# Performance work log

Measured on AMD Instinct MI355X. Metric: run time of the kernel, lower is better.

Reference implementation:

```python
import jax, jax.numpy as jnp
import numpy as np

HID = 64

def _rnn_layer(x, W_ih, W_hh, b_ih, b_hh):
    # x: [B, T, F]; PyTorch RNN step: h_t = tanh(x_t @ W_ih.T + b_ih + h_{t-1} @ W_hh.T + b_hh)
    # Precompute the input projection for all timesteps as one big GEMM.
    x_proj = jnp.einsum('btf,hf->bth', x, W_ih) + b_ih  # [B, T, H]
    B = x.shape[0]
    h0 = jnp.zeros((B, HID), x.dtype)

    def step(h, xt):
        h = jnp.tanh(xt + h @ W_hh.T + b_hh)
        return h, h

    _, hs = jax.lax.scan(step, h0, jnp.swapaxes(x_proj, 0, 1))  # hs: [T, B, H]
    return jnp.swapaxes(hs, 0, 1)  # [B, T, H]


def setup_inputs() -> dict:
    key = jax.random.key(0)
    ks = jax.random.split(key, 20)
    B, T, F = 4096, 128, 14
    s_in = 1.0 / np.sqrt(HID)  # PyTorch RNN init scale
    d = {
        'x': jax.random.normal(ks[0], (B, T, F), jnp.float32),
        'W_ih0': jax.random.normal(ks[1], (HID, F), jnp.float32) * s_in,
        'W_hh0': jax.random.normal(ks[2], (HID, HID), jnp.float32) * s_in,
        'b_ih0': jax.random.normal(ks[3], (HID,), jnp.float32) * s_in,
        'b_hh0': jax.random.normal(ks[4], (HID,), jnp.float32) * s_in,
        'W_ih1': jax.random.normal(ks[5], (HID, HID), jnp.float32) * s_in,
        'W_hh1': jax.random.normal(ks[6], (HID, HID), jnp.float32) * s_in,
        'b_ih1': jax.random.normal(ks[7], (HID,), jnp.float32) * s_in,
        'b_hh1': jax.random.normal(ks[8], (HID,), jnp.float32) * s_in,
        'W_ih2': jax.random.normal(ks[9], (HID, HID), jnp.float32) * s_in,
        'W_hh2': jax.random.normal(ks[10], (HID, HID), jnp.float32) * s_in,
        'b_ih2': jax.random.normal(ks[11], (HID,), jnp.float32) * s_in,
        'b_hh2': jax.random.normal(ks[12], (HID,), jnp.float32) * s_in,
        'fc1_w': jax.random.normal(ks[13], (32, HID), jnp.float32) * s_in,
        'fc1_b': jax.random.normal(ks[14], (32,), jnp.float32) * s_in,
        'fc2_w': jax.random.normal(ks[15], (1, 32), jnp.float32) * (1.0 / np.sqrt(32)),
        'fc2_b': jax.random.normal(ks[16], (1,), jnp.float32) * (1.0 / np.sqrt(32)),
    }
    return d


def reference(x, W_ih0, W_hh0, b_ih0, b_hh0, W_ih1, W_hh1, b_ih1, b_hh1,
              W_ih2, W_hh2, b_ih2, b_hh2, fc1_w, fc1_b, fc2_w, fc2_b):
    h = _rnn_layer(x, W_ih0, W_hh0, b_ih0, b_hh0)
    h = _rnn_layer(h, W_ih1, W_hh1, b_ih1, b_hh1)
    h = _rnn_layer(h, W_ih2, W_hh2, b_ih2, b_hh2)
    last = h[:, -1, :]                       # [B, H]
    y = jax.nn.relu(last @ fc1_w.T + fc1_b)  # [B, 32]
    return y @ fc2_w.T + fc2_b               # [B, 1]
```

## Files before the change

kernel.cpp:

```cpp
#include <hip/hip_runtime.h>

typedef short  s16x8 __attribute__((ext_vector_type(8)));
typedef float  f32x4 __attribute__((ext_vector_type(4)));
typedef float  f32x2 __attribute__((ext_vector_type(2)));
typedef unsigned int u32;
typedef unsigned int u32x4 __attribute__((ext_vector_type(4)));
typedef unsigned short u16;

#define DEVI static __device__ __forceinline__

#if __has_builtin(__builtin_amdgcn_exp2f)
#define EXP2(v) __builtin_amdgcn_exp2f(v)
#else
#define EXP2(v) exp2f(v)
#endif

constexpr int T_  = 128;
constexpr int F_  = 14;
constexpr int H_  = 64;
constexpr int BPB = 16;
constexpr int K_  = 4;
constexpr int NCH = T_ / K_;

constexpr int HF_BYTES   = 2 * 2 * K_ * 2 * 64 * 16;
constexpr int XBUF_BYTES = 2 * K_ * 64 * 16;
constexpr int QBUF_BYTES = 2 * 3 * K_ * 4 * 64 * 16;
constexpr int SMEM_BYTES = HF_BYTES + XBUF_BYTES + QBUF_BYTES;

DEVI u16 f2bf(float f) {
  u32 u = __builtin_bit_cast(u32, f);
  u += 0x7fffu + ((u >> 16) & 1u);
  return (u16)(u >> 16);
}
DEVI u32 cvtpk(float a, float b) {
  u32 r;
  asm("v_cvt_pk_bf16_f32 %0, %1, %2" : "=v"(r) : "v"(a), "v"(b));
  return r;
}
DEVI s16x8 packfrag(const f32x4& a, const f32x4& b) {
  u32x4 p;
  p[0] = cvtpk(a[0], a[1]); p[1] = cvtpk(a[2], a[3]);
  p[2] = cvtpk(b[0], b[1]); p[3] = cvtpk(b[2], b[3]);
  return __builtin_bit_cast(s16x8, p);
}
DEVI f32x4 tanh4(const f32x4& v) {
  const f32x4 kC = -2.8853900817779268f;
  f32x4 t = v * kC;
  f32x4 e;
  e[0] = EXP2(t[0]); e[1] = EXP2(t[1]);
  e[2] = EXP2(t[2]); e[3] = EXP2(t[3]);
  const f32x4 kOne = 1.0f;
  f32x4 d = e + kOne;
  f32x4 r;
  r[0] = __builtin_amdgcn_rcpf(d[0]); r[1] = __builtin_amdgcn_rcpf(d[1]);
  r[2] = __builtin_amdgcn_rcpf(d[2]); r[3] = __builtin_amdgcn_rcpf(d[3]);
  const f32x4 kTwo = 2.0f, kNegOne = -1.0f;
  return __builtin_elementwise_fma(kTwo, r, kNegOne);
}
DEVI f32x4 MFMA(s16x8 a, s16x8 b, f32x4 c) {
  return __builtin_amdgcn_mfma_f32_16x16x32_bf16(a, b, c, 0, 0, 0);
}
DEVI s16x8 ldrow8(const float* p) {
  const f32x4 a = ((const f32x4*)p)[0];
  const f32x4 b = ((const f32x4*)p)[1];
  s16x8 r;
  r[0] = (short)f2bf(a[0]); r[1] = (short)f2bf(a[1]);
  r[2] = (short)f2bf(a[2]); r[3] = (short)f2bf(a[3]);
  r[4] = (short)f2bf(b[0]); r[5] = (short)f2bf(b[1]);
  r[6] = (short)f2bf(b[2]); r[7] = (short)f2bf(b[3]);
  return r;
}

__global__ __launch_bounds__(512, 1) void rnn_ck(
    const float* __restrict__ x,
    const float* __restrict__ Wih0, const float* __restrict__ Whh0,
    const float* __restrict__ bih0, const float* __restrict__ bhh0,
    const float* __restrict__ Wih1, const float* __restrict__ Whh1,
    const float* __restrict__ bih1, const float* __restrict__ bhh1,
    const float* __restrict__ Wih2, const float* __restrict__ Whh2,
    const float* __restrict__ bih2, const float* __restrict__ bhh2,
    const float* __restrict__ fc1w, const float* __restrict__ fc1b,
    const float* __restrict__ fc2w, const float* __restrict__ fc2b,
    float* __restrict__ out)
{
  extern __shared__ __align__(16) char smem[];
  u32x4 (*hf)[2][K_][2][64]   = (u32x4 (*)[2][K_][2][64])smem;
  u32x4 (*xbuf)[K_][64]       = (u32x4 (*)[K_][64])(smem + HF_BYTES);
  f32x4 (*qbuf)[3][K_][4][64] = (f32x4 (*)[3][K_][4][64])(smem + HF_BYTES + XBUF_BYTES);

  const int tid  = threadIdx.x;
  const int wv   = tid >> 6;
  const int lane = tid & 63;
  const int g    = lane >> 4;
  const int m    = lane & 15;
  const int b0   = blockIdx.x * BPB;

  const bool isB = (wv < 3);
  const bool isP = (wv == 3);
  const bool isA = (wv >= 4 && wv < 7);
  const int  l   = isB ? wv : (wv - 4);

  f32x4 z4; z4[0] = 0.f; z4[1] = 0.f; z4[2] = 0.f; z4[3] = 0.f;
  s16x8 zf;
  #pragma unroll
  for (int i = 0; i < 8; i++) zf[i] = 0;

  s16x8 Ax[4], Ai[4][2], Ah[4][2];
  f32x4 bc[4];
  if (isB) {
    const float* Wh = (l == 0) ? Whh0 : (l == 1) ? Whh1 : Whh2;
    #pragma unroll
    for (int n = 0; n < 4; n++) {
      const int Lr = 32 * (n & 1) + 8 * (m >> 2) + 4 * (n >> 1) + (m & 3);
      Ah[n][0] = ldrow8(Wh + Lr * H_ + 8 * g);
      Ah[n][1] = ldrow8(Wh + Lr * H_ + 32 + 8 * g);
    }
  } else if (isA) {
    const float* Wi = (l == 1) ? Wih1 : Wih2;
    const float* bi = (l == 0) ? bih0 : (l == 1) ? bih1 : bih2;
    const float* bh = (l == 0) ? bhh0 : (l == 1) ? bhh1 : bhh2;
    #pragma unroll
    for (int n = 0; n < 4; n++) {
      const int Lr = 32 * (n & 1) + 8 * (m >> 2) + 4 * (n >> 1) + (m & 3);
      if (l == 0) {
        s16x8 r;
        #pragma unroll
        for (int j2 = 0; j2 < 8; j2++) {
          const int kk = 8 * g + j2;
          r[j2] = (kk < F_) ? (short)f2bf(Wih0[Lr * F_ + kk]) : (short)0;
        }
        Ax[n] = r;
      } else {
        Ai[n][0] = ldrow8(Wi + Lr * H_ + 8 * g);
        Ai[n][1] = ldrow8(Wi + Lr * H_ + 32 + 8 * g);
      }
      const int Lb = 32 * (n & 1) + 8 * g + 4 * (n >> 1);
      bc[n] = *(const f32x4*)(bi + Lb) + *(const f32x4*)(bh + Lb);
    }
  }

  s16x8 F[2];
  F[0] = zf; F[1] = zf;
  f32x4 h2v[4];
  #pragma unroll
  for (int n = 0; n < 4; n++) h2v[n] = z4;

  const float* xrow = x + (size_t)(b0 + m) * T_ * F_;
  auto ldraw = [&](int t, f32x4& ra, f32x4& rb) {
    const float* p = xrow + t * F_;
    if (g == 0) {
      f32x2 p0 = *(const f32x2*)(p),     p1 = *(const f32x2*)(p + 2);
      f32x2 p2 = *(const f32x2*)(p + 4), p3 = *(const f32x2*)(p + 6);
      ra[0] = p0[0]; ra[1] = p0[1]; ra[2] = p1[0]; ra[3] = p1[1];
      rb[0] = p2[0]; rb[1] = p2[1]; rb[2] = p3[0]; rb[3] = p3[1];
    } else if (g == 1) {
      f32x2 p4 = *(const f32x2*)(p + 8), p5 = *(const f32x2*)(p + 10);
      f32x2 p6 = *(const f32x2*)(p + 12);
      ra[0] = p4[0]; ra[1] = p4[1]; ra[2] = p5[0]; ra[3] = p5[1];
      rb[0] = p6[0]; rb[1] = p6[1]; rb[2] = 0.f;   rb[3] = 0.f;
    } else {
      ra = z4; rb = z4;
    }
  };
  auto cvtraw = [&](const f32x4& ra, const f32x4& rb) -> s16x8 {
    u32x4 p;
    p[0] = cvtpk(ra[0], ra[1]); p[1] = cvtpk(ra[2], ra[3]);
    p[2] = cvtpk(rb[0], rb[1]); p[3] = cvtpk(rb[2], rb[3]);
    return __builtin_bit_cast(s16x8, p);
  };
  auto stage4 = [&](int par, int t0) {
    f32x4 ra[K_], rb[K_];
    #pragma unroll
    for (int k = 0; k < K_; k++) ldraw(t0 + k, ra[k], rb[k]);
    #pragma unroll
    for (int k = 0; k < K_; k++)
      xbuf[par][k][lane] = __builtin_bit_cast(u32x4, cvtraw(ra[k], rb[k]));
  };

  if (isP) stage4(0, 0);
  __syncthreads();

  #pragma unroll 1
  for (int e = 0; e < NCH + 6; e++) {
    const int wb = e & 1, rbuf = wb ^ 1;

    if (isP) {
      if (e >= 1 && e < NCH) stage4(wb, e * K_);
    } else if (isA) {
      const int c = e - (2 * l + 1);
      if (c >= 0 && c < NCH) {
        if (l == 0) {
          #pragma unroll
          for (int k = 0; k < K_; k++) {
            const s16x8 xf = __builtin_bit_cast(s16x8, xbuf[rbuf][k][lane]);
            #pragma unroll
            for (int n = 0; n < 4; n++)
              qbuf[wb][0][k][n][lane] = MFMA(Ax[n], xf, bc[n]);
          }
        } else {
          #pragma unroll
          for (int k = 0; k < K_; k++) {
            const s16x8 P0 = __builtin_bit_cast(s16x8, hf[rbuf][l - 1][k][0][lane]);
            const s16x8 P1 = __builtin_bit_cast(s16x8, hf[rbuf][l - 1][k][1][lane]);
            f32x4 q[4];
            #pragma unroll
            for (int n = 0; n < 4; n++) q[n] = MFMA(Ai[n][0], P0, bc[n]);
            #pragma unroll
            for (int n = 0; n < 4; n++) q[n] = MFMA(Ai[n][1], P1, q[n]);
            #pragma unroll
            for (int n = 0; n < 4; n++) qbuf[wb][l][k][n][lane] = q[n];
          }
        }
      }
    } else if (isB) {
      const int c = e - (2 * l + 2);
      if (c >= 0 && c < NCH) {
        #pragma unroll
        for (int k = 0; k < K_; k++) {
          const f32x4 qc0 = qbuf[rbuf][l][k][0][lane];
          const f32x4 qc1 = qbuf[rbuf][l][k][1][lane];
          const f32x4 qc2 = qbuf[rbuf][l][k][2][lane];
          const f32x4 qc3 = qbuf[rbuf][l][k][3][lane];
          f32x4 p[4];
          p[0] = MFMA(Ah[0][0], F[0], qc0);
          p[2] = MFMA(Ah[2][0], F[0], qc2);
          p[1] = MFMA(Ah[1][0], F[0], qc1);
          p[3] = MFMA(Ah[3][0], F[0], qc3);
          p[0] = MFMA(Ah[0][1], F[1], p[0]);
          p[2] = MFMA(Ah[2][1], F[1], p[2]);
          p[1] = MFMA(Ah[1][1], F[1], p[1]);
          p[3] = MFMA(Ah[3][1], F[1], p[3]);

          f32x4 hv0 = tanh4(p[0]);
          f32x4 hv2 = tanh4(p[2]);
          F[0] = packfrag(hv0, hv2);
          f32x4 hv1 = tanh4(p[1]);
          f32x4 hv3 = tanh4(p[3]);
          F[1] = packfrag(hv1, hv3);

          if (l < 2) {
            hf[wb][l][k][0][lane] = __builtin_bit_cast(u32x4, F[0]);
            hf[wb][l][k][1][lane] = __builtin_bit_cast(u32x4, F[1]);
          } else if (c == NCH - 1 && k == K_ - 1) {
            h2v[0] = hv0; h2v[1] = hv1;
            h2v[2] = hv2; h2v[3] = hv3;
          }
        }
      }
    }
    __syncthreads();
  }

  float (*h2l)[68] = (float (*)[68])smem;
  if (wv == 2) {
    #pragma unroll
    for (int n = 0; n < 4; n++) {
      const int Lb = 32 * (n & 1) + 8 * g + 4 * (n >> 1);
      *(f32x4*)&h2l[m][Lb] = h2v[n];
    }
  }
  __syncthreads();

  if (wv == 0) {
    float hr[64];
    #pragma unroll
    for (int q = 0; q < 16; q++) {
      f32x4 v = *(const f32x4*)&h2l[m][4 * q];
      hr[4 * q + 0] = v[0]; hr[4 * q + 1] = v[1];
      hr[4 * q + 2] = v[2]; hr[4 * q + 3] = v[3];
    }
    float acc2 = 0.f;
    #pragma unroll
    for (int jj = 0; jj < 8; jj++) {
      const int jf = 8 * g + jj;
      float s = fc1b[jf];
      const f32x4* wp = (const f32x4*)(fc1w + jf * H_);
      #pragma unroll
      for (int kq = 0; kq < 16; kq++) {
        f32x4 wv2 = wp[kq];
        s += hr[4 * kq + 0] * wv2[0] + hr[4 * kq + 1] * wv2[1]
           + hr[4 * kq + 2] * wv2[2] + hr[4 * kq + 3] * wv2[3];
      }
      s = fmaxf(s, 0.f);
      acc2 += s * fc2w[jf];
    }
    acc2 += __shfl_xor(acc2, 16, 64);
    acc2 += __shfl_xor(acc2, 32, 64);
    if (lane < 16) out[b0 + m] = acc2 + fc2b[0];
  }
}

extern "C" void kernel_launch(void* const* d_in, const int* in_sizes, int n_in,
                              void* d_out, int out_size, void* d_ws, size_t ws_size,
                              hipStream_t stream) {
  const float* x    = (const float*)d_in[0];
  const float* Wih0 = (const float*)d_in[1];
  const float* Whh0 = (const float*)d_in[2];
  const float* bih0 = (const float*)d_in[3];
  const float* bhh0 = (const float*)d_in[4];
  const float* Wih1 = (const float*)d_in[5];
  const float* Whh1 = (const float*)d_in[6];
  const float* bih1 = (const float*)d_in[7];
  const float* bhh1 = (const float*)d_in[8];
  const float* Wih2 = (const float*)d_in[9];
  const float* Whh2 = (const float*)d_in[10];
  const float* bih2 = (const float*)d_in[11];
  const float* bhh2 = (const float*)d_in[12];
  const float* fc1w = (const float*)d_in[13];
  const float* fc1b = (const float*)d_in[14];
  const float* fc2w = (const float*)d_in[15];
  const float* fc2b = (const float*)d_in[16];

  static bool s_attr_set = false;
  if (!s_attr_set) {
    (void)hipFuncSetAttribute((const void*)rnn_ck,
                              hipFuncAttributeMaxDynamicSharedMemorySize,
                              SMEM_BYTES);
    s_attr_set = true;
  }

  rnn_ck<<<dim3(4096 / BPB), dim3(512), SMEM_BYTES, stream>>>(
      x, Wih0, Whh0, bih0, bhh0, Wih1, Whh1, bih1, bhh1,
      Wih2, Whh2, bih2, bhh2, fc1w, fc1b, fc2w, fc2b, (float*)d_out);
}
```

Before: 160.7 us.

## Merge three recurrent-layer waves into one interleaved wave and shrink block to 320

Result: slower. 222.9 us (+38.7%).

```diff
diff --git a/kernel.cpp b/kernel.cpp
--- a/kernel.cpp
+++ b/kernel.cpp
@@ -71,7 +71,7 @@
   return r;
 }
 
-__global__ __launch_bounds__(512, 1) void rnn_ck(
+__global__ __launch_bounds__(320, 1) void rnn_ck(
     const float* __restrict__ x,
     const float* __restrict__ Wih0, const float* __restrict__ Whh0,
     const float* __restrict__ bih0, const float* __restrict__ bhh0,
@@ -95,34 +95,34 @@
   const int m    = lane & 15;
   const int b0   = blockIdx.x * BPB;
 
-  const bool isB = (wv < 3);
-  const bool isP = (wv == 3);
-  const bool isA = (wv >= 4 && wv < 7);
-  const int  l   = isB ? wv : (wv - 4);
-
   f32x4 z4; z4[0] = 0.f; z4[1] = 0.f; z4[2] = 0.f; z4[3] = 0.f;
   s16x8 zf;
   #pragma unroll
   for (int i = 0; i < 8; i++) zf[i] = 0;
 
-  s16x8 Ax[4], Ai[4][2], Ah[4][2];
+  s16x8 Ah[3][4][2];
+  s16x8 Ax[4], Ai[4][2];
   f32x4 bc[4];
-  if (isB) {
-    const float* Wh = (l == 0) ? Whh0 : (l == 1) ? Whh1 : Whh2;
+  if (wv == 0) {
+    const float* Whs[3] = {Whh0, Whh1, Whh2};
+    #pragma unroll
+    for (int l = 0; l < 3; l++) {
+      #pragma unroll
+      for (int n = 0; n < 4; n++) {
+        const int Lr = 32 * (n & 1) + 8 * (m >> 2) + 4 * (n >> 1) + (m & 3);
+        Ah[l][n][0] = ldrow8(Whs[l] + Lr * H_ + 8 * g);
+        Ah[l][n][1] = ldrow8(Whs[l] + Lr * H_ + 32 + 8 * g);
+      }
+    }
+  } else if (wv >= 2) {
+    const int al = wv - 2;
+    const float* Wi = (al == 1) ? Wih1 : Wih2;
+    const float* bi = (al == 0) ? bih0 : (al == 1) ? bih1 : bih2;
+    const float* bh = (al == 0) ? bhh0 : (al == 1) ? bhh1 : bhh2;
     #pragma unroll
     for (int n = 0; n < 4; n++) {
       const int Lr = 32 * (n & 1) + 8 * (m >> 2) + 4 * (n >> 1) + (m & 3);
-      Ah[n][0] = ldrow8(Wh + Lr * H_ + 8 * g);
-      Ah[n][1] = ldrow8(Wh + Lr * H_ + 32 + 8 * g);
-    }
-  } else if (isA) {
-    const float* Wi = (l == 1) ? Wih1 : Wih2;
-    const float* bi = (l == 0) ? bih0 : (l == 1) ? bih1 : bih2;
-    const float* bh = (l == 0) ? bhh0 : (l == 1) ? bhh1 : bhh2;
-    #pragma unroll
-    for (int n = 0; n < 4; n++) {
-      const int Lr = 32 * (n & 1) + 8 * (m >> 2) + 4 * (n >> 1) + (m & 3);
-      if (l == 0) {
+      if (al == 0) {
         s16x8 r;
         #pragma unroll
         for (int j2 = 0; j2 < 8; j2++) {
@@ -139,8 +139,9 @@
     }
   }
 
-  s16x8 F[2];
-  F[0] = zf; F[1] = zf;
+  s16x8 F[3][2];
+  #pragma unroll
+  for (int l = 0; l < 3; l++) { F[l][0] = zf; F[l][1] = zf; }
   f32x4 h2v[4];
   #pragma unroll
   for (int n = 0; n < 4; n++) h2v[n] = z4;
@@ -177,22 +178,74 @@
       xbuf[par][k][lane] = __builtin_bit_cast(u32x4, cvtraw(ra[k], rb[k]));
   };
 
-  if (isP) stage4(0, 0);
+  auto stepL = [&](int l, int kk, int cl, int rbuf) {
+    const f32x4 qc0 = qbuf[rbuf][l][kk][0][lane];
+    const f32x4 qc1 = qbuf[rbuf][l][kk][1][lane];
+    const f32x4 qc2 = qbuf[rbuf][l][kk][2][lane];
+    const f32x4 qc3 = qbuf[rbuf][l][kk][3][lane];
+    f32x4 p[4];
+    p[0] = MFMA(Ah[l][0][0], F[l][0], qc0);
+    p[2] = MFMA(Ah[l][2][0], F[l][0], qc2);
+    p[1] = MFMA(Ah[l][1][0], F[l][0], qc1);
+    p[3] = MFMA(Ah[l][3][0], F[l][0], qc3);
+    p[0] = MFMA(Ah[l][0][1], F[l][1], p[0]);
+    p[2] = MFMA(Ah[l][2][1], F[l][1], p[2]);
+    p[1] = MFMA(Ah[l][1][1], F[l][1], p[1]);
+    p[3] = MFMA(Ah[l][3][1], F[l][1], p[3]);
+
+    f32x4 hv0 = tanh4(p[0]);
+    f32x4 hv2 = tanh4(p[2]);
+    F[l][0] = packfrag(hv0, hv2);
+    f32x4 hv1 = tanh4(p[1]);
+    f32x4 hv3 = tanh4(p[3]);
+    F[l][1] = packfrag(hv1, hv3);
+
+    if (l < 2) {
+      hf[cl & 1][l][kk][0][lane] = __builtin_bit_cast(u32x4, F[l][0]);
+      hf[cl & 1][l][kk][1][lane] = __builtin_bit_cast(u32x4, F[l][1]);
+    } else if (cl == NCH - 1 && kk == K_ - 1) {
+      h2v[0] = hv0; h2v[1] = hv1;
+      h2v[2] = hv2; h2v[3] = hv3;
+    }
+  };
+
+  if (wv == 1) stage4(0, 0);
   __syncthreads();
 
   #pragma unroll 1
-  for (int e = 0; e < NCH + 6; e++) {
+  for (int e = 0; e < NCH + 5; e++) {
     const int wb = e & 1, rbuf = wb ^ 1;
 
-    if (isP) {
-      if (e >= 1 && e < NCH) stage4(wb, e * K_);
-    } else if (isA) {
-      const int c = e - (2 * l + 1);
+    if (wv == 0) {
+      const int c0 = e - 1, c1 = e - 3, c2 = e - 5;
+      if (e >= 5 && e <= NCH) {
+        #pragma unroll
+        for (int kk = 0; kk < K_; kk++) {
+          stepL(0, kk, c0, rbuf);
+          stepL(1, kk, c1, rbuf);
+          stepL(2, kk, c2, rbuf);
+        }
+      } else {
+        const bool a0 = (c0 >= 0) && (c0 < NCH);
+        const bool a1 = (c1 >= 0) && (c1 < NCH);
+        const bool a2 = (c2 >= 0) && (c2 < NCH);
+        #pragma unroll
+        for (int kk = 0; kk < K_; kk++) {
+          if (a0) stepL(0, kk, c0, rbuf);
+          if (a1) stepL(1, kk, c1, rbuf);
+          if (a2) stepL(2, kk, c2, rbuf);
+        }
+      }
+    } else if (wv == 1) {
+      if (e <= NCH - 2) stage4(rbuf, (e + 1) * K_);
+    } else {
+      const int al = wv - 2;
+      const int c  = e - 2 * al;
       if (c >= 0 && c < NCH) {
-        if (l == 0) {
+        if (al == 0) {
           #pragma unroll
           for (int k = 0; k < K_; k++) {
-            const s16x8 xf = __builtin_bit_cast(s16x8, xbuf[rbuf][k][lane]);
+            const s16x8 xf = __builtin_bit_cast(s16x8, xbuf[wb][k][lane]);
             #pragma unroll
             for (int n = 0; n < 4; n++)
               qbuf[wb][0][k][n][lane] = MFMA(Ax[n], xf, bc[n]);
@@ -200,59 +253,24 @@
         } else {
           #pragma unroll
           for (int k = 0; k < K_; k++) {
-            const s16x8 P0 = __builtin_bit_cast(s16x8, hf[rbuf][l - 1][k][0][lane]);
-            const s16x8 P1 = __builtin_bit_cast(s16x8, hf[rbuf][l - 1][k][1][lane]);
+            const s16x8 P0 = __builtin_bit_cast(s16x8, hf[wb][al - 1][k][0][lane]);
+            const s16x8 P1 = __builtin_bit_cast(s16x8, hf[wb][al - 1][k][1][lane]);
             f32x4 q[4];
             #pragma unroll
             for (int n = 0; n < 4; n++) q[n] = MFMA(Ai[n][0], P0, bc[n]);
             #pragma unroll
             for (int n = 0; n < 4; n++) q[n] = MFMA(Ai[n][1], P1, q[n]);
             #pragma unroll
-            for (int n = 0; n < 4; n++) qbuf[wb][l][k][n][lane] = q[n];
+            for (int n = 0; n < 4; n++) qbuf[wb][al][k][n][lane] = q[n];
           }
         }
       }
-    } else if (isB) {
-      const int c = e - (2 * l + 2);
-      if (c >= 0 && c < NCH) {
-        #pragma unroll
-        for (int k = 0; k < K_; k++) {
-          const f32x4 qc0 = qbuf[rbuf][l][k][0][lane];
-          const f32x4 qc1 = qbuf[rbuf][l][k][1][lane];
-          const f32x4 qc2 = qbuf[rbuf][l][k][2][lane];
-          const f32x4 qc3 = qbuf[rbuf][l][k][3][lane];
-          f32x4 p[4];
-          p[0] = MFMA(Ah[0][0], F[0], qc0);
-          p[2] = MFMA(Ah[2][0], F[0], qc2);
-          p[1] = MFMA(Ah[1][0], F[0], qc1);
-          p[3] = MFMA(Ah[3][0], F[0], qc3);
-          p[0] = MFMA(Ah[0][1], F[1], p[0]);
-          p[2] = MFMA(Ah[2][1], F[1], p[2]);
-          p[1] = MFMA(Ah[1][1], F[1], p[1]);
-          p[3] = MFMA(Ah[3][1], F[1], p[3]);
-
-          f32x4 hv0 = tanh4(p[0]);
-          f32x4 hv2 = tanh4(p[2]);
-          F[0] = packfrag(hv0, hv2);
-          f32x4 hv1 = tanh4(p[1]);
-          f32x4 hv3 = tanh4(p[3]);
-          F[1] = packfrag(hv1, hv3);
-
-          if (l < 2) {
-            hf[wb][l][k][0][lane] = __builtin_bit_cast(u32x4, F[0]);
-            hf[wb][l][k][1][lane] = __builtin_bit_cast(u32x4, F[1]);
-          } else if (c == NCH - 1 && k == K_ - 1) {
-            h2v[0] = hv0; h2v[1] = hv1;
-            h2v[2] = hv2; h2v[3] = hv3;
-          }
-        }
-      }
     }
     __syncthreads();
   }
 
   float (*h2l)[68] = (float (*)[68])smem;
-  if (wv == 2) {
+  if (wv == 0) {
     #pragma unroll
     for (int n = 0; n < 4; n++) {
       const int Lb = 32 * (n & 1) + 8 * g + 4 * (n >> 1);
@@ -319,7 +337,7 @@
     s_attr_set = true;
   }
 
-  rnn_ck<<<dim3(4096 / BPB), dim3(512), SMEM_BYTES, stream>>>(
+  rnn_ck<<<dim3(4096 / BPB), dim3(320), SMEM_BYTES, stream>>>(
       x, Wih0, Whh0, bih0, bhh0, Wih1, Whh1, bih1, bhh1,
       Wih2, Whh2, bih2, bhh2, fc1w, fc1b, fc2w, fc2b, (float*)d_out);
 }
```
